# Optimization experiments

Hardware: AMD Instinct MI355X
Metric: run time of the kernel (lower is better)

## Reference

```python
import jax, jax.numpy as jnp
import numpy as np

B, T, V, E, H = 64, 512, 32000, 256, 256


def _gru_scan(xp, h0, rkernel, rbias):
    # xp: [T,B,3H] precomputed input projections (incl. input bias)
    # Keras GRUCell with reset_after=True semantics.
    def step(h, xpt):
        hp = h @ rkernel + rbias            # [B,3H]
        xz, xr, xh = jnp.split(xpt, 3, axis=-1)
        hz, hr, hh = jnp.split(hp, 3, axis=-1)
        z = jax.nn.sigmoid(xz + hz)
        r = jax.nn.sigmoid(xr + hr)
        hc = jnp.tanh(xh + r * hh)
        hn = z * h + (1.0 - z) * hc
        return hn, hn
    return jax.lax.scan(step, h0, xp)


def setup_inputs() -> dict:
    key = jax.random.key(0)
    ks = jax.random.split(key, 8)
    s_in = 1.0 / np.sqrt(E)
    s_rec = 1.0 / np.sqrt(H)
    return {
        "x": jax.random.randint(ks[0], (B, T), 0, V, dtype=jnp.int32),
        "hidden": jnp.zeros((B, H), jnp.float32),
        "emb": jax.random.normal(ks[1], (V, E), jnp.float32) * 0.05,
        "kernel_f": jax.random.normal(ks[2], (E, 3 * H), jnp.float32) * s_in,
        "rkernel_f": jax.random.normal(ks[3], (H, 3 * H), jnp.float32) * s_rec,
        "bias_f": jnp.zeros((2, 3 * H), jnp.float32),
        "kernel_b": jax.random.normal(ks[4], (E, 3 * H), jnp.float32) * s_in,
        "rkernel_b": jax.random.normal(ks[5], (H, 3 * H), jnp.float32) * s_rec,
        "bias_b": jnp.zeros((2, 3 * H), jnp.float32),
    }


def reference(x, hidden, emb, kernel_f, rkernel_f, bias_f, kernel_b, rkernel_b, bias_b):
    e = emb[x]                                   # [B,T,E] embedding lookup

    def run(kernel, rkernel, bias, reverse):
        xp = jnp.einsum('bte,eh->tbh', e, kernel) + bias[0]  # [T,B,3H]
        if reverse:
            xp = xp[::-1]
        hT, ys = _gru_scan(xp, hidden, rkernel, bias[1])
        ys = jnp.swapaxes(ys, 0, 1)              # [B,T,H]
        if reverse:
            ys = ys[:, ::-1]
        return hT, ys

    h_f, y_f = run(kernel_f, rkernel_f, bias_f, False)
    h_b, y_b = run(kernel_b, rkernel_b, bias_b, True)
    concatenated = jnp.concatenate([y_f, y_b], axis=-1)  # [B,T,2H]
    return concatenated, h_f, h_b
```

## Files before the change

### kernel.cpp

```cpp
#include <hip/hip_runtime.h>
#include <hip/hip_bf16.h>

typedef _Float16 h2v __attribute__((ext_vector_type(2)));

#define B_SZ 64
#define T_SZ 512
#define E_SZ 256
#define H_SZ 256
#define C_SZ 768

__device__ __forceinline__ float dot2f(h2v a, h2v b, float c) {
#if __has_builtin(__builtin_amdgcn_fdot2)
  return __builtin_amdgcn_fdot2(a, b, c, false);
#else
  return c + (float)a[0] * (float)b[0] + (float)a[1] * (float)b[1];
#endif
}

__device__ __forceinline__ float rcp_fast(float x) {
  return __builtin_amdgcn_rcpf(x);
}

__global__ __launch_bounds__(256) void xp_gemm_kernel(
    const int* __restrict__ x,
    const float* __restrict__ emb,
    const float* __restrict__ kf, const float* __restrict__ bf,
    const float* __restrict__ kb, const float* __restrict__ bb,
    _Float16* __restrict__ xp)
{
  const int ct  = blockIdx.x;
  const int rt  = blockIdx.y;
  const int dir = blockIdx.z;
  const float* Kp = dir ? kb : kf;
  const float* Bp = dir ? bb : bf;
  const int c0 = ct * 48;
  const int r0 = rt * 64;
  const int tid = threadIdx.x;

  __shared__ __align__(16) _Float16 As[64][264];
  __shared__ __align__(16) _Float16 Bs[48][264];

  for (int r = 0; r < 64; ++r) {
    int xi = x[r0 + r];
    As[r][tid] = (_Float16)emb[(size_t)xi * E_SZ + tid];
  }
  for (int i = tid; i < 48 * 256; i += 256) {
    int k = i / 48;
    int c = i - k * 48;
    Bs[c][k] = (_Float16)Kp[k * C_SZ + c0 + c];
  }
  __syncthreads();

  const int tr = tid >> 4;
  const int tc = tid & 15;
  float acc[4][3];
  #pragma unroll
  for (int i = 0; i < 4; ++i)
    #pragma unroll
    for (int j = 0; j < 3; ++j) acc[i][j] = 0.f;

  #pragma unroll
  for (int m = 0; m < 32; ++m) {
    float4 a4[4], b4[3];
    #pragma unroll
    for (int i = 0; i < 4; ++i) a4[i] = *(const float4*)&As[tr * 4 + i][m * 8];
    #pragma unroll
    for (int j = 0; j < 3; ++j) b4[j] = *(const float4*)&Bs[tc + 16 * j][m * 8];
    #pragma unroll
    for (int i = 0; i < 4; ++i) {
      const h2v* ah = (const h2v*)&a4[i];
      #pragma unroll
      for (int j = 0; j < 3; ++j) {
        const h2v* bh = (const h2v*)&b4[j];
        #pragma unroll
        for (int p = 0; p < 4; ++p) acc[i][j] = dot2f(ah[p], bh[p], acc[i][j]);
      }
    }
  }

  #pragma unroll
  for (int j = 0; j < 3; ++j) {
    int c = c0 + tc + 16 * j;
    float bias = Bp[c];
    #pragma unroll
    for (int i = 0; i < 4; ++i) {
      int r = r0 + tr * 4 + i;
      xp[((size_t)dir * (B_SZ * T_SZ) + r) * C_SZ + c] = (_Float16)(acc[i][j] + bias);
    }
  }
}

__global__ __launch_bounds__(768, 3) void gru_scan_kernel(
    const float* __restrict__ hidden,
    const float* __restrict__ rkf, const float* __restrict__ bf,
    const float* __restrict__ rkb, const float* __restrict__ bb,
    const _Float16* __restrict__ xp,
    float* __restrict__ out)
{
  const int b   = blockIdx.x;
  const int dir = blockIdx.y;
  const int j   = threadIdx.x;
  const float* RK = dir ? rkb : rkf;
  const float* BS = dir ? bb : bf;

  __shared__ __align__(16) _Float16 hbuf[H_SZ];
  __shared__ __align__(16) float hp[C_SZ];

  h2v col[128];
  #pragma unroll
  for (int kk = 0; kk < 128; ++kk) {
    float f0 = RK[(2 * kk) * C_SZ + j];
    float f1 = RK[(2 * kk + 1) * C_SZ + j];
    h2v c2;
    c2[0] = (_Float16)f0;
    c2[1] = (_Float16)f1;
    col[kk] = c2;
  }
  const float rb = BS[C_SZ + j];

  float hreg = 0.f;
  if (j < H_SZ) {
    hreg = hidden[b * H_SZ + j];
    hbuf[j] = (_Float16)hreg;
  }

  const size_t xbase = ((size_t)dir * (B_SZ * T_SZ) + (size_t)b * T_SZ) * C_SZ;
  float xz_c = 0.f, xr_c = 0.f, xh_c = 0.f;
  if (j < H_SZ) {
    int t0 = dir ? (T_SZ - 1) : 0;
    const _Float16* xr0 = xp + xbase + (size_t)t0 * C_SZ;
    xz_c = (float)xr0[j];
    xr_c = (float)xr0[j + H_SZ];
    xh_c = (float)xr0[j + 2 * H_SZ];
  }
  __syncthreads();

  for (int s = 0; s < T_SZ; ++s) {
    float xz_n = 0.f, xr_n = 0.f, xh_n = 0.f;
    if (j < H_SZ) {
      int sn = (s + 1 < T_SZ) ? (s + 1) : s;
      int tn = dir ? (T_SZ - 1 - sn) : sn;
      const _Float16* xrn = xp + xbase + (size_t)tn * C_SZ;
      xz_n = (float)xrn[j];
      xr_n = (float)xrn[j + H_SZ];
      xh_n = (float)xrn[j + 2 * H_SZ];
    }

    float acc = rb;
    const float4* hb4 = (const float4*)hbuf;
    #pragma unroll
    for (int m = 0; m < 32; ++m) {
      float4 q = hb4[m];
      const h2v* hq = (const h2v*)&q;
      acc = dot2f(hq[0], col[4 * m + 0], acc);
      acc = dot2f(hq[1], col[4 * m + 1], acc);
      acc = dot2f(hq[2], col[4 * m + 2], acc);
      acc = dot2f(hq[3], col[4 * m + 3], acc);
    }
    hp[j] = acc;
    __syncthreads();

    if (j < H_SZ) {
      float z  = rcp_fast(1.f + __expf(-(xz_c + hp[j])));
      float r  = rcp_fast(1.f + __expf(-(xr_c + hp[j + H_SZ])));
      float pre = xh_c + r * hp[j + 2 * H_SZ];
      float e2 = __expf(2.f * pre);
      float hc = 1.f - 2.f * rcp_fast(e2 + 1.f);
      hreg = z * hreg + (1.f - z) * hc;
      int t = dir ? (T_SZ - 1 - s) : s;
      out[((size_t)b * T_SZ + t) * (2 * H_SZ) + dir * H_SZ + j] = hreg;
      hbuf[j] = (_Float16)hreg;
    }
    __syncthreads();

    xz_c = xz_n; xr_c = xr_n; xh_c = xh_n;
  }

  if (j < H_SZ) {
    out[(size_t)(B_SZ * T_SZ) * (2 * H_SZ) + dir * (B_SZ * H_SZ) + b * H_SZ + j] = hreg;
  }
}

extern "C" void kernel_launch(void* const* d_in, const int* in_sizes, int n_in,
                              void* d_out, int out_size, void* d_ws, size_t ws_size,
                              hipStream_t stream) {
  const int*   x    = (const int*)d_in[0];
  const float* hid  = (const float*)d_in[1];
  const float* emb  = (const float*)d_in[2];
  const float* kf   = (const float*)d_in[3];
  const float* rkf  = (const float*)d_in[4];
  const float* bf   = (const float*)d_in[5];
  const float* kb   = (const float*)d_in[6];
  const float* rkb  = (const float*)d_in[7];
  const float* bb   = (const float*)d_in[8];
  float* out = (float*)d_out;

  _Float16* xp = (_Float16*)d_ws;

  dim3 g1(16, 512, 2);
  xp_gemm_kernel<<<g1, 256, 0, stream>>>(x, emb, kf, bf, kb, bb, xp);

  dim3 g2(B_SZ, 2);
  gru_scan_kernel<<<g2, 768, 0, stream>>>(hid, rkf, bf, rkb, bb, xp, out);
}
```

Before: 1.126 ms.

## Split GRU recurrent dot product across lane quads with DPP reduction

Changes the recurrent matvec in the scan kernel so each group of 4 lanes covers 4 output columns, with each lane taking one quarter of the K dimension. Partial sums are combined with DPP quad shuffles and each lane then picks its own column. Each lane now reads a quarter of the hidden vector from LDS per step instead of all of it, and the buffer is padded to avoid bank conflicts, so LDS traffic on the serial critical path drops. In exchange it adds DPP adds and selects, and changes the register-pressure hint to waves_per_eu(3,3).

```diff
diff --git a/kernel.cpp b/kernel.cpp
--- a/kernel.cpp
+++ b/kernel.cpp
@@ -19,6 +19,17 @@
 
 __device__ __forceinline__ float rcp_fast(float x) {
   return __builtin_amdgcn_rcpf(x);
+}
+
+__device__ __forceinline__ float dpp_add_x1(float v) {
+  int i = __builtin_bit_cast(int, v);
+  int s = __builtin_amdgcn_update_dpp(i, i, 0xB1, 0xF, 0xF, true);
+  return v + __builtin_bit_cast(float, s);
+}
+__device__ __forceinline__ float dpp_add_x2(float v) {
+  int i = __builtin_bit_cast(int, v);
+  int s = __builtin_amdgcn_update_dpp(i, i, 0x4E, 0xF, 0xF, true);
+  return v + __builtin_bit_cast(float, s);
 }
 
 __global__ __launch_bounds__(256) void xp_gemm_kernel(
@@ -90,7 +101,8 @@
   }
 }
 
-__global__ __launch_bounds__(768, 3) void gru_scan_kernel(
+__global__ __launch_bounds__(768) __attribute__((amdgpu_waves_per_eu(3, 3)))
+void gru_scan_kernel(
     const float* __restrict__ hidden,
     const float* __restrict__ rkf, const float* __restrict__ bf,
     const float* __restrict__ rkb, const float* __restrict__ bb,
@@ -99,85 +111,100 @@
 {
   const int b   = blockIdx.x;
   const int dir = blockIdx.y;
-  const int j   = threadIdx.x;
+  const int tid = threadIdx.x;
+  const int q   = tid & 3;
   const float* RK = dir ? rkb : rkf;
   const float* BS = dir ? bb : bf;
 
-  __shared__ __align__(16) _Float16 hbuf[H_SZ];
+  __shared__ __align__(16) _Float16 hbuf[4 * 72];
   __shared__ __align__(16) float hp[C_SZ];
 
-  h2v col[128];
-  #pragma unroll
-  for (int kk = 0; kk < 128; ++kk) {
-    float f0 = RK[(2 * kk) * C_SZ + j];
-    float f1 = RK[(2 * kk + 1) * C_SZ + j];
-    h2v c2;
-    c2[0] = (_Float16)f0;
-    c2[1] = (_Float16)f1;
-    col[kk] = c2;
-  }
-  const float rb = BS[C_SZ + j];
+  h2v col[4][32];
+  const int cbase = tid & ~3;
+  #pragma unroll
+  for (int o = 0; o < 4; ++o) {
+    #pragma unroll
+    for (int m = 0; m < 32; ++m) {
+      int k = 64 * q + 2 * m;
+      h2v c2;
+      c2[0] = (_Float16)RK[(size_t)k * C_SZ + cbase + o];
+      c2[1] = (_Float16)RK[(size_t)(k + 1) * C_SZ + cbase + o];
+      col[o][m] = c2;
+    }
+  }
+  const float rb = BS[C_SZ + tid];
 
   float hreg = 0.f;
-  if (j < H_SZ) {
-    hreg = hidden[b * H_SZ + j];
-    hbuf[j] = (_Float16)hreg;
+  if (tid < H_SZ) {
+    hreg = hidden[b * H_SZ + tid];
+    hbuf[72 * (tid >> 6) + (tid & 63)] = (_Float16)hreg;
   }
 
   const size_t xbase = ((size_t)dir * (B_SZ * T_SZ) + (size_t)b * T_SZ) * C_SZ;
   float xz_c = 0.f, xr_c = 0.f, xh_c = 0.f;
-  if (j < H_SZ) {
+  if (tid < H_SZ) {
     int t0 = dir ? (T_SZ - 1) : 0;
     const _Float16* xr0 = xp + xbase + (size_t)t0 * C_SZ;
-    xz_c = (float)xr0[j];
-    xr_c = (float)xr0[j + H_SZ];
-    xh_c = (float)xr0[j + 2 * H_SZ];
+    xz_c = (float)xr0[tid];
+    xr_c = (float)xr0[tid + H_SZ];
+    xh_c = (float)xr0[tid + 2 * H_SZ];
   }
   __syncthreads();
 
   for (int s = 0; s < T_SZ; ++s) {
     float xz_n = 0.f, xr_n = 0.f, xh_n = 0.f;
-    if (j < H_SZ) {
+    if (tid < H_SZ) {
       int sn = (s + 1 < T_SZ) ? (s + 1) : s;
       int tn = dir ? (T_SZ - 1 - sn) : sn;
       const _Float16* xrn = xp + xbase + (size_t)tn * C_SZ;
-      xz_n = (float)xrn[j];
-      xr_n = (float)xrn[j + H_SZ];
-      xh_n = (float)xrn[j + 2 * H_SZ];
-    }
-
-    float acc = rb;
-    const float4* hb4 = (const float4*)hbuf;
-    #pragma unroll
-    for (int m = 0; m < 32; ++m) {
-      float4 q = hb4[m];
-      const h2v* hq = (const h2v*)&q;
-      acc = dot2f(hq[0], col[4 * m + 0], acc);
-      acc = dot2f(hq[1], col[4 * m + 1], acc);
-      acc = dot2f(hq[2], col[4 * m + 2], acc);
-      acc = dot2f(hq[3], col[4 * m + 3], acc);
-    }
-    hp[j] = acc;
+      xz_n = (float)xrn[tid];
+      xr_n = (float)xrn[tid + H_SZ];
+      xh_n = (float)xrn[tid + 2 * H_SZ];
+    }
+
+    float acc0 = 0.f, acc1 = 0.f, acc2 = 0.f, acc3 = 0.f;
+    const float4* hsl = (const float4*)(hbuf + 72 * q);
+    #pragma unroll
+    for (int i = 0; i < 8; ++i) {
+      float4 c = hsl[i];
+      const h2v* hv = (const h2v*)&c;
+      #pragma unroll
+      for (int p = 0; p < 4; ++p) {
+        int m = 4 * i + p;
+        acc0 = dot2f(hv[p], col[0][m], acc0);
+        acc1 = dot2f(hv[p], col[1][m], acc1);
+        acc2 = dot2f(hv[p], col[2][m], acc2);
+        acc3 = dot2f(hv[p], col[3][m], acc3);
+      }
+    }
+    acc0 = dpp_add_x2(dpp_add_x1(acc0));
+    acc1 = dpp_add_x2(dpp_add_x1(acc1));
+    acc2 = dpp_add_x2(dpp_add_x1(acc2));
+    acc3 = dpp_add_x2(dpp_add_x1(acc3));
+    float sel01 = (q & 1) ? acc1 : acc0;
+    float sel23 = (q & 1) ? acc3 : acc2;
+    float val   = (q & 2) ? sel23 : sel01;
+    hp[tid] = val + rb;
     __syncthreads();
 
-    if (j < H_SZ) {
-      float z  = rcp_fast(1.f + __expf(-(xz_c + hp[j])));
-      float r  = rcp_fast(1.f + __expf(-(xr_c + hp[j + H_SZ])));
-      float pre = xh_c + r * hp[j + 2 * H_SZ];
+    if (tid < H_SZ) {
+      float z  = rcp_fast(1.f + __expf(-(xz_c + hp[tid])));
+      float r  = rcp_fast(1.f + __expf(-(xr_c + hp[tid + H_SZ])));
+      float pre = xh_c + r * hp[tid + 2 * H_SZ];
       float e2 = __expf(2.f * pre);
       float hc = 1.f - 2.f * rcp_fast(e2 + 1.f);
       hreg = z * hreg + (1.f - z) * hc;
       int t = dir ? (T_SZ - 1 - s) : s;
-      out[((size_t)b * T_SZ + t) * (2 * H_SZ) + dir * H_SZ + j] = hreg;
-      hbuf[j] = (_Float16)hreg;
+      out[((size_t)b * T_SZ + t) * (2 * H_SZ) + dir * H_SZ + tid] = hreg;
+      hbuf[72 * (tid >> 6) + (tid & 63)] = (_Float16)hreg;
     }
     __syncthreads();
 
     xz_c = xz_n; xr_c = xr_n; xh_c = xh_n;
   }
 
-  if (j < H_SZ) {
-    out[(size_t)(B_SZ * T_SZ) * (2 * H_SZ) + dir * (B_SZ * H_SZ) + b * H_SZ + j] = hreg;
+  if (tid < H_SZ) {
+    out[(size_t)(B_SZ * T_SZ) * (2 * H_SZ) + dir * (B_SZ * H_SZ) + b * H_SZ + tid] = hreg;
   }
 }
 
```

New measurement: 1.100 ms. 1.02x faster.
